# Kernel optimization log

Measured on AMD Instinct MI355X. Metric: run time of the kernel, lower is better.

Reference implementation:

```python
import jax, jax.numpy as jnp
import numpy as np
import math

DIM = 512


def setup_inputs() -> dict:
    key = jax.random.key(0)
    ks = jax.random.split(key, 6)
    B, N, D = 4, 4096, DIM
    H = D // 2
    features = jax.random.normal(ks[0], (B, N, D), dtype=jnp.float32)
    W1 = jax.random.normal(ks[1], (D, H), dtype=jnp.float32) * 0.02
    b1 = jnp.zeros((H,), dtype=jnp.float32)
    ln_g = jnp.ones((H,), dtype=jnp.float32)
    ln_b = jnp.zeros((H,), dtype=jnp.float32)
    W2 = jax.random.normal(ks[2], (H, 1), dtype=jnp.float32) * 0.02
    b2 = jnp.zeros((1,), dtype=jnp.float32)
    target_entropy = jnp.ones((1,), dtype=jnp.float32) * math.log(D)
    temperature = jnp.ones((1,), dtype=jnp.float32)
    return {"features": features, "W1": W1, "b1": b1, "ln_g": ln_g,
            "ln_b": ln_b, "W2": W2, "b2": b2,
            "target_entropy": target_entropy, "temperature": temperature}


def _layernorm(x, g, b, eps=1e-5):
    mu = jnp.mean(x, axis=-1, keepdims=True)
    var = jnp.mean((x - mu) ** 2, axis=-1, keepdims=True)
    return (x - mu) * jax.lax.rsqrt(var + eps) * g + b


def reference(features, W1, b1, ln_g, ln_b, W2, b2, target_entropy, temperature):
    # ---- compute_entropy: pairwise RBF kernel over [B, N, D] ----
    sq = jnp.sum(features ** 2, axis=-1)                       # [B, N]
    gram = jnp.einsum('bnd,bmd->bnm', features, features)      # [B, N, N]
    d2 = jnp.maximum(sq[:, :, None] + sq[:, None, :] - 2.0 * gram, 0.0)
    tau = temperature[0]
    kernel = jnp.exp(-d2 / (2.0 * tau ** 2))                   # [B, N, N]
    probs = kernel / jnp.sum(kernel, axis=-1, keepdims=True)
    entropy = -jnp.sum(probs * jnp.log(probs + 1e-6), axis=-1)  # [B, N]

    # ---- entropy estimator MLP (computed in original forward, output unused) ----
    h = features @ W1 + b1
    h = _layernorm(h, ln_g, ln_b)
    h = jax.nn.gelu(h, approximate=False)
    estimated_entropy = h @ W2 + b2                            # [B, N, 1] (unused)
    del estimated_entropy

    # ---- sigmoid-gated control signal ----
    entropy_diff = entropy - target_entropy[0]
    control_signal = jax.nn.sigmoid(-entropy_diff / tau)       # [B, N]
    controlled_features = features * control_signal[..., None]
    return controlled_features, control_signal
```

## Files before the change

### kernel.cpp

```cpp
#include <hip/hip_runtime.h>
#include <stdint.h>

#define N_TOK 4096
#define DIM   512
#define BATCH 4
#define BN    (BATCH * N_TOK)
#define JSPLIT 8
#define IPW   64
#define IPB   256
#define NG    (N_TOK / JSPLIT / 16)

typedef __attribute__((ext_vector_type(4))) float f32x4;
typedef __attribute__((ext_vector_type(8))) int   i32x8;

__device__ __forceinline__ float sumsq8(uint lo, uint hi) {
    float s = 0.f, f;
    f = __builtin_amdgcn_cvt_f32_fp8((int)lo, 0); s = fmaf(f, f, s);
    f = __builtin_amdgcn_cvt_f32_fp8((int)lo, 1); s = fmaf(f, f, s);
    f = __builtin_amdgcn_cvt_f32_fp8((int)lo, 2); s = fmaf(f, f, s);
    f = __builtin_amdgcn_cvt_f32_fp8((int)lo, 3); s = fmaf(f, f, s);
    f = __builtin_amdgcn_cvt_f32_fp8((int)hi, 0); s = fmaf(f, f, s);
    f = __builtin_amdgcn_cvt_f32_fp8((int)hi, 1); s = fmaf(f, f, s);
    f = __builtin_amdgcn_cvt_f32_fp8((int)hi, 2); s = fmaf(f, f, s);
    f = __builtin_amdgcn_cvt_f32_fp8((int)hi, 3); s = fmaf(f, f, s);
    return s;
}

__global__ __launch_bounds__(256) void prep_kernel(
    const float* __restrict__ feat, uint8_t* __restrict__ fb,
    uint8_t* __restrict__ fbT, float* __restrict__ sq)
{
    __shared__ __align__(16) long lt[1024];
    const int t = threadIdx.x;
    const int row16 = t >> 4, seg = t & 15;
    const size_t grp = blockIdx.x;
    const size_t row = grp * 16 + row16;

    const float4* src = (const float4*)(feat + row * DIM + seg * 32);
    uint32_t wd[8];
    float s = 0.f;
#pragma unroll
    for (int i = 0; i < 4; ++i) {
        float4 a = src[2 * i], b = src[2 * i + 1];
        uint lo = (uint)__builtin_amdgcn_cvt_pk_fp8_f32(a.x, a.y, 0, false);
        lo      = (uint)__builtin_amdgcn_cvt_pk_fp8_f32(a.z, a.w, (int)lo, true);
        uint hi = (uint)__builtin_amdgcn_cvt_pk_fp8_f32(b.x, b.y, 0, false);
        hi      = (uint)__builtin_amdgcn_cvt_pk_fp8_f32(b.z, b.w, (int)hi, true);
        wd[2 * i] = lo; wd[2 * i + 1] = hi;
        s += sumsq8(lo, hi);
    }

    uint4* dst = (uint4*)(fb + row * DIM + seg * 32);
    uint4 o0; o0.x = wd[0]; o0.y = wd[1]; o0.z = wd[2]; o0.w = wd[3];
    uint4 o1; o1.x = wd[4]; o1.y = wd[5]; o1.z = wd[6]; o1.w = wd[7];
    dst[0] = o0; dst[1] = o1;

#pragma unroll
    for (int i = 0; i < 4; ++i) {
        int c = seg * 4 + i;
        long d = ((long)(unsigned)wd[2 * i + 1] << 32) | (unsigned)wd[2 * i];
        lt[c * 16 + ((row16 + c) & 15)] = d;
    }

#pragma unroll
    for (int m = 1; m < 16; m <<= 1) s += __shfl_xor(s, m);
    if (seg == 0) sq[row] = s;

    __syncthreads();
    long* ot = (long*)(fbT + grp * 8192);
#pragma unroll
    for (int i = 0; i < 4; ++i) {
        int p   = t + i * 256;
        int kk  = p >> 8;
        int rem = p & 255;
        int q   = rem >> 6;
        int r   = (rem >> 2) & 15;
        int w8  = p & 3;
        int c   = kk * 16 + q * 4 + w8;
        ot[p] = lt[c * 16 + ((r + c) & 15)];
    }
}

__global__ __launch_bounds__(256, 2) void entropy_kernel(
    const uint8_t* __restrict__ fb, const uint8_t* __restrict__ fbT,
    const float* __restrict__ sq, const float* __restrict__ temp,
    float* __restrict__ Sp, float* __restrict__ Tp)
{
    const int t    = threadIdx.x;
    const int w    = t >> 6;
    const int lane = t & 63;
    const int q    = lane >> 4;
    const int c16  = lane & 15;

    const int flat  = blockIdx.x;
    const int combo = flat & 31;
    const int batch = combo >> 3;
    const int jh    = combo & 7;
    const int iblk  = flat >> 5;
    const int iw    = iblk * IPB + w * IPW;
    const size_t rowbase = (size_t)batch * N_TOK;

    const float tau    = temp[0];
    const float inv2t2 = 0.5f / (tau * tau);
    const float cg     = 1.0f / (tau * tau);

    i32x8 afrag[4][4];
#pragma unroll
    for (int s = 0; s < 4; ++s) {
        const uint4* ap = (const uint4*)(fb + (rowbase + iw + s * 16 + c16) * DIM);
#pragma unroll
        for (int kk = 0; kk < 4; ++kk) {
            uint4 lo = ap[kk * 8 + q * 2];
            uint4 hi = ap[kk * 8 + q * 2 + 1];
            i32x8 v = {(int)lo.x, (int)lo.y, (int)lo.z, (int)lo.w,
                       (int)hi.x, (int)hi.y, (int)hi.z, (int)hi.w};
            afrag[s][kk] = v;
        }
    }
    float pi[4][4];
#pragma unroll
    for (int s = 0; s < 4; ++s)
#pragma unroll
        for (int r = 0; r < 4; ++r)
            pi[s][r] = -sq[rowbase + iw + s * 16 + q * 4 + r] * inv2t2;

    float S[4][4], T[4][4];
#pragma unroll
    for (int s = 0; s < 4; ++s)
#pragma unroll
        for (int r = 0; r < 4; ++r) { S[s][r] = 0.f; T[s][r] = 0.f; }

    const uint4* bp = (const uint4*)(fbT
                    + ((size_t)batch * (N_TOK / 16) + (size_t)jh * NG) * 8192)
                    + q * 32 + c16 * 2;
    const float* sqj = sq + rowbase + jh * (N_TOK / JSPLIT) + c16;

    for (int g = 0; g < NG; ++g) {
        float pj = -sqj[g * 16] * inv2t2;
        const uint4* bg = bp + (size_t)g * 512;
        f32x4 acc[4] = {{0,0,0,0},{0,0,0,0},{0,0,0,0},{0,0,0,0}};
#pragma unroll
        for (int kk = 0; kk < 4; kk += 2) {
            uint4 l0 = bg[kk * 128],       h0 = bg[kk * 128 + 1];
            uint4 l1 = bg[(kk+1) * 128],   h1 = bg[(kk+1) * 128 + 1];
            i32x8 b0 = {(int)l0.x, (int)l0.y, (int)l0.z, (int)l0.w,
                        (int)h0.x, (int)h0.y, (int)h0.z, (int)h0.w};
            i32x8 b1 = {(int)l1.x, (int)l1.y, (int)l1.z, (int)l1.w,
                        (int)h1.x, (int)h1.y, (int)h1.z, (int)h1.w};
            acc[0] = __builtin_amdgcn_mfma_scale_f32_16x16x128_f8f6f4(afrag[0][kk], b0, acc[0], 0, 0, 0, 127, 0, 127);
            acc[1] = __builtin_amdgcn_mfma_scale_f32_16x16x128_f8f6f4(afrag[1][kk], b0, acc[1], 0, 0, 0, 127, 0, 127);
            acc[2] = __builtin_amdgcn_mfma_scale_f32_16x16x128_f8f6f4(afrag[2][kk], b0, acc[2], 0, 0, 0, 127, 0, 127);
            acc[3] = __builtin_amdgcn_mfma_scale_f32_16x16x128_f8f6f4(afrag[3][kk], b0, acc[3], 0, 0, 0, 127, 0, 127);
            acc[0] = __builtin_amdgcn_mfma_scale_f32_16x16x128_f8f6f4(afrag[0][kk+1], b1, acc[0], 0, 0, 0, 127, 0, 127);
            acc[1] = __builtin_amdgcn_mfma_scale_f32_16x16x128_f8f6f4(afrag[1][kk+1], b1, acc[1], 0, 0, 0, 127, 0, 127);
            acc[2] = __builtin_amdgcn_mfma_scale_f32_16x16x128_f8f6f4(afrag[2][kk+1], b1, acc[2], 0, 0, 0, 127, 0, 127);
            acc[3] = __builtin_amdgcn_mfma_scale_f32_16x16x128_f8f6f4(afrag[3][kk+1], b1, acc[3], 0, 0, 0, 127, 0, 127);
        }
        float m = -1e30f;
#pragma unroll
        for (int s = 0; s < 4; ++s)
#pragma unroll
            for (int r = 0; r < 4; ++r) {
                acc[s][r] = fmaf(acc[s][r], cg, pi[s][r] + pj);
                m = fmaxf(m, acc[s][r]);
            }
        if (m > -110.0f) {
#pragma unroll
            for (int s = 0; s < 4; ++s)
#pragma unroll
                for (int r = 0; r < 4; ++r) {
                    float ee = fminf(acc[s][r], 0.f);
                    float k  = __expf(ee);
                    S[s][r] += k;
                    T[s][r]  = fmaf(k, ee, T[s][r]);
                }
        }
    }

#pragma unroll
    for (int m = 1; m < 16; m <<= 1)
#pragma unroll
        for (int s = 0; s < 4; ++s)
#pragma unroll
            for (int r = 0; r < 4; ++r) {
                S[s][r] += __shfl_xor(S[s][r], m);
                T[s][r] += __shfl_xor(T[s][r], m);
            }

    if (c16 == 0) {
#pragma unroll
        for (int s = 0; s < 4; ++s)
#pragma unroll
            for (int r = 0; r < 4; ++r) {
                size_t idx = (size_t)jh * BN + rowbase + iw + s * 16 + q * 4 + r;
                Sp[idx] = S[s][r];
                Tp[idx] = T[s][r];
            }
    }
}

__global__ __launch_bounds__(256) void finalize_kernel(
    const float* __restrict__ feat, const float* __restrict__ Sp,
    const float* __restrict__ Tp, const float* __restrict__ tgt,
    const float* __restrict__ temp, float* __restrict__ out)
{
    int row  = (blockIdx.x << 2) + (threadIdx.x >> 6);
    int lane = threadIdx.x & 63;
    float S = 0.0f, T = 0.0f;
#pragma unroll
    for (int j = 0; j < JSPLIT; ++j) {
        S += Sp[(size_t)j * BN + row];
        T += Tp[(size_t)j * BN + row];
    }
    float tau = temp[0];
    float E  = __logf(S) - T / S;
    float cs = 1.0f / (1.0f + __expf((E - tgt[0]) / tau));

    const float4* F4 = (const float4*)(feat + (size_t)row * DIM);
    float4*       O4 = (float4*)(out + (size_t)row * DIM);
    float4 v0 = F4[lane], v1 = F4[lane + 64];
    v0.x *= cs; v0.y *= cs; v0.z *= cs; v0.w *= cs;
    v1.x *= cs; v1.y *= cs; v1.z *= cs; v1.w *= cs;
    O4[lane] = v0; O4[lane + 64] = v1;
    if (lane == 0) out[(size_t)BN * DIM + row] = cs;
}

extern "C" void kernel_launch(void* const* d_in, const int* in_sizes, int n_in,
                              void* d_out, int out_size, void* d_ws, size_t ws_size,
                              hipStream_t stream) {
    const float* feat = (const float*)d_in[0];
    const float* tgt  = (const float*)d_in[7];
    const float* temp = (const float*)d_in[8];
    float* out = (float*)d_out;

    char* ws = (char*)d_ws;
    uint8_t* fb  = (uint8_t*)ws;
    uint8_t* fbT = fb + (size_t)BN * DIM;
    float*   sq  = (float*)(fbT + (size_t)BN * DIM);
    float*   Sp  = sq + BN;
    float*   Tp  = Sp + (size_t)JSPLIT * BN;

    prep_kernel<<<dim3(BN / 16), dim3(256), 0, stream>>>(feat, fb, fbT, sq);
    entropy_kernel<<<dim3((N_TOK / IPB) * BATCH * JSPLIT), dim3(256), 0, stream>>>(fb, fbT, sq, temp, Sp, Tp);
    finalize_kernel<<<dim3(BN / 4), dim3(256), 0, stream>>>(feat, Sp, Tp, tgt, temp, out);
}
```

Baseline: 157.7 us.

## Stage B tiles through double-buffered LDS with async global_load_lds

Each block now cooperatively loads the shared 8KB fp8 B tile for the next j-group straight into a double-buffered LDS array using global_load_lds. Every wave then reads its MFMA operands from LDS instead of issuing its own global loads. The prep kernel's transposed layout is reordered so the tile matches the 16-byte-per-lane LDS copy pattern. This removes the four-fold redundant global traffic across waves and overlaps the next tile's fetch with compute, at the cost of a __syncthreads per iteration and 16KB of LDS per block.

```diff
diff --git a/kernel.cpp b/kernel.cpp
--- a/kernel.cpp
+++ b/kernel.cpp
@@ -12,6 +12,9 @@
 
 typedef __attribute__((ext_vector_type(4))) float f32x4;
 typedef __attribute__((ext_vector_type(8))) int   i32x8;
+
+typedef const __attribute__((address_space(1))) uint32_t* gptr_t;
+typedef __attribute__((address_space(3))) uint32_t* lptr_t;
 
 __device__ __forceinline__ float sumsq8(uint lo, uint hi) {
     float s = 0.f, f;
@@ -70,13 +73,15 @@
     long* ot = (long*)(fbT + grp * 8192);
 #pragma unroll
     for (int i = 0; i < 4; ++i) {
-        int p   = t + i * 256;
-        int kk  = p >> 8;
-        int rem = p & 255;
-        int q   = rem >> 6;
-        int r   = (rem >> 2) & 15;
-        int w8  = p & 3;
-        int c   = kk * 16 + q * 4 + w8;
+        int p    = t + i * 256;
+        int kk   = p >> 8;
+        int rem  = p & 255;
+        int half = rem >> 7;
+        int l6   = (rem >> 1) & 63;
+        int qq   = l6 >> 4;
+        int r    = l6 & 15;
+        int w8   = half * 2 + (p & 1);
+        int c    = kk * 16 + qq * 4 + w8;
         ot[p] = lt[c * 16 + ((r + c) & 15)];
     }
 }
@@ -86,11 +91,13 @@
     const float* __restrict__ sq, const float* __restrict__ temp,
     float* __restrict__ Sp, float* __restrict__ Tp)
 {
+    __shared__ uint4 Bs[2][512];
     const int t    = threadIdx.x;
     const int w    = t >> 6;
     const int lane = t & 63;
     const int q    = lane >> 4;
     const int c16  = lane & 15;
+    const int lbo  = lane * 16;
 
     const int flat  = blockIdx.x;
     const int combo = flat & 31;
@@ -130,31 +137,43 @@
 #pragma unroll
         for (int r = 0; r < 4; ++r) { S[s][r] = 0.f; T[s][r] = 0.f; }
 
-    const uint4* bp = (const uint4*)(fbT
-                    + ((size_t)batch * (N_TOK / 16) + (size_t)jh * NG) * 8192)
-                    + q * 32 + c16 * 2;
+    const uint8_t* bgbase = fbT
+        + ((size_t)batch * (N_TOK / 16) + (size_t)jh * NG) * 8192;
     const float* sqj = sq + rowbase + jh * (N_TOK / JSPLIT) + c16;
 
+    {
+        const uint8_t* gs = bgbase + w * 2048 + lbo;
+        uint8_t* ld = (uint8_t*)Bs[0] + w * 2048;
+        __builtin_amdgcn_global_load_lds((gptr_t)(const void*)gs,
+                                         (lptr_t)(void*)ld, 16, 0, 0);
+        __builtin_amdgcn_global_load_lds((gptr_t)(const void*)(gs + 1024),
+                                         (lptr_t)(void*)(ld + 1024), 16, 0, 0);
+    }
+    __syncthreads();
+
+    int cur = 0;
     for (int g = 0; g < NG; ++g) {
-        float pj = -sqj[g * 16] * inv2t2;
-        const uint4* bg = bp + (size_t)g * 512;
+        if (g + 1 < NG) {
+            const uint8_t* gs = bgbase + (size_t)(g + 1) * 8192 + w * 2048 + lbo;
+            uint8_t* ld = (uint8_t*)Bs[cur ^ 1] + w * 2048;
+            __builtin_amdgcn_global_load_lds((gptr_t)(const void*)gs,
+                                             (lptr_t)(void*)ld, 16, 0, 0);
+            __builtin_amdgcn_global_load_lds((gptr_t)(const void*)(gs + 1024),
+                                             (lptr_t)(void*)(ld + 1024), 16, 0, 0);
+        }
+        float pj = -sqj[(size_t)g * 16] * inv2t2;
+        const uint8_t* bs = (const uint8_t*)Bs[cur];
         f32x4 acc[4] = {{0,0,0,0},{0,0,0,0},{0,0,0,0},{0,0,0,0}};
 #pragma unroll
-        for (int kk = 0; kk < 4; kk += 2) {
-            uint4 l0 = bg[kk * 128],       h0 = bg[kk * 128 + 1];
-            uint4 l1 = bg[(kk+1) * 128],   h1 = bg[(kk+1) * 128 + 1];
-            i32x8 b0 = {(int)l0.x, (int)l0.y, (int)l0.z, (int)l0.w,
-                        (int)h0.x, (int)h0.y, (int)h0.z, (int)h0.w};
-            i32x8 b1 = {(int)l1.x, (int)l1.y, (int)l1.z, (int)l1.w,
-                        (int)h1.x, (int)h1.y, (int)h1.z, (int)h1.w};
-            acc[0] = __builtin_amdgcn_mfma_scale_f32_16x16x128_f8f6f4(afrag[0][kk], b0, acc[0], 0, 0, 0, 127, 0, 127);
-            acc[1] = __builtin_amdgcn_mfma_scale_f32_16x16x128_f8f6f4(afrag[1][kk], b0, acc[1], 0, 0, 0, 127, 0, 127);
-            acc[2] = __builtin_amdgcn_mfma_scale_f32_16x16x128_f8f6f4(afrag[2][kk], b0, acc[2], 0, 0, 0, 127, 0, 127);
-            acc[3] = __builtin_amdgcn_mfma_scale_f32_16x16x128_f8f6f4(afrag[3][kk], b0, acc[3], 0, 0, 0, 127, 0, 127);
-            acc[0] = __builtin_amdgcn_mfma_scale_f32_16x16x128_f8f6f4(afrag[0][kk+1], b1, acc[0], 0, 0, 0, 127, 0, 127);
-            acc[1] = __builtin_amdgcn_mfma_scale_f32_16x16x128_f8f6f4(afrag[1][kk+1], b1, acc[1], 0, 0, 0, 127, 0, 127);
-            acc[2] = __builtin_amdgcn_mfma_scale_f32_16x16x128_f8f6f4(afrag[2][kk+1], b1, acc[2], 0, 0, 0, 127, 0, 127);
-            acc[3] = __builtin_amdgcn_mfma_scale_f32_16x16x128_f8f6f4(afrag[3][kk+1], b1, acc[3], 0, 0, 0, 127, 0, 127);
+        for (int kk = 0; kk < 4; ++kk) {
+            uint4 lo = *(const uint4*)(bs + kk * 2048 + lbo);
+            uint4 hi = *(const uint4*)(bs + kk * 2048 + 1024 + lbo);
+            i32x8 b = {(int)lo.x, (int)lo.y, (int)lo.z, (int)lo.w,
+                       (int)hi.x, (int)hi.y, (int)hi.z, (int)hi.w};
+            acc[0] = __builtin_amdgcn_mfma_scale_f32_16x16x128_f8f6f4(afrag[0][kk], b, acc[0], 0, 0, 0, 127, 0, 127);
+            acc[1] = __builtin_amdgcn_mfma_scale_f32_16x16x128_f8f6f4(afrag[1][kk], b, acc[1], 0, 0, 0, 127, 0, 127);
+            acc[2] = __builtin_amdgcn_mfma_scale_f32_16x16x128_f8f6f4(afrag[2][kk], b, acc[2], 0, 0, 0, 127, 0, 127);
+            acc[3] = __builtin_amdgcn_mfma_scale_f32_16x16x128_f8f6f4(afrag[3][kk], b, acc[3], 0, 0, 0, 127, 0, 127);
         }
         float m = -1e30f;
 #pragma unroll
@@ -175,6 +194,8 @@
                     T[s][r]  = fmaf(k, ee, T[s][r]);
                 }
         }
+        __syncthreads();
+        cur ^= 1;
     }
 
 #pragma unroll
```

New measurement: 150.0 us. 4.9% less time.
